# Performance work log

Hardware: AMD Instinct MI355X
Metric: run time of the kernel (lower is better)

Reference implementation:

```python
import jax, jax.numpy as jnp
import numpy as np

N = 50000      # nodes
E = 800000     # edges (avg degree 16)
IN, EMB, HID, OUT = 128, 256, 256, 128
KS = (25000, 12500)  # absolute top-k node counts per pooling level
NEG = -1e9


def setup_inputs() -> dict:
    key = jax.random.key(0)
    k = jax.random.split(key, 20)
    s = 0.05
    rn = lambda kk, shp: (jax.random.normal(kk, shp, jnp.float32) * s)
    return {
        "features": jax.random.normal(k[0], (N, IN), jnp.float32),
        "src": jax.random.randint(k[1], (E,), 0, N, dtype=jnp.int32),
        "dst": jax.random.randint(k[2], (E,), 0, N, dtype=jnp.int32),
        "W_embed": rn(k[3], (IN, EMB)), "b_embed": jnp.zeros((EMB,), jnp.float32),
        "W_enc0": rn(k[4], (EMB, HID)), "b_enc0": jnp.zeros((HID,), jnp.float32),
        "W_enc1": rn(k[5], (HID, HID)), "b_enc1": jnp.zeros((HID,), jnp.float32),
        "W_p0": rn(k[6], (HID, 1)), "b_p0": jnp.zeros((1,), jnp.float32),
        "W_p1": rn(k[7], (HID, 1)), "b_p1": jnp.zeros((1,), jnp.float32),
        "W_bot": rn(k[8], (HID, HID)), "b_bot": jnp.zeros((HID,), jnp.float32),
        "W_dec0": rn(k[9], (HID, HID)), "b_dec0": jnp.zeros((HID,), jnp.float32),
        "W_dec1": rn(k[10], (HID, OUT)), "b_dec1": jnp.zeros((OUT,), jnp.float32),
    }


def _gcn(h, src, dst, emask, W, b, act):
    """DGL GraphConv, norm='both': D_out^{-1/2} A D_in^{-1/2} h W + b, deg clamped >=1.
    emask: float [E] validity mask for edges of the current (sub)graph."""
    n = h.shape[0]
    deg_out = jnp.clip(jax.ops.segment_sum(emask, src, num_segments=n), 1.0)
    deg_in = jnp.clip(jax.ops.segment_sum(emask, dst, num_segments=n), 1.0)
    msg = (h * (deg_out ** -0.5)[:, None])[src] * emask[:, None]  # [E, F]
    agg = jax.ops.segment_sum(msg, dst, num_segments=n)
    out = (agg * (deg_in ** -0.5)[:, None]) @ W + b
    return jax.nn.relu(out) if act else out


def _forward(features, src, dst, W_embed, b_embed, W_enc0, b_enc0, W_enc1, b_enc1,
             W_p0, b_p0, W_p1, b_p1, W_bot, b_bot, W_dec0, b_dec0, W_dec1, b_dec1):
    n = features.shape[0]
    ones_e = jnp.ones((src.shape[0],), features.dtype)
    enc = [(W_enc0, b_enc0), (W_enc1, b_enc1)]
    pools = [(W_p0, b_p0), (W_p1, b_p1)]
    dec = [(W_dec0, b_dec0), (W_dec1, b_dec1)]
    L = len(KS)

    h = _gcn(features, src, dst, ones_e, W_embed, b_embed, True)
    masks = [jnp.ones((n,), features.dtype)]  # node mask per graph level
    hidden = []
    for i in range(L):  # encoder (dropout = eval-mode identity)
        m = masks[i]
        em = m[src] * m[dst]
        h = _gcn(h, src, dst, em, enc[i][0], enc[i][1], True) * m[:, None]
        hidden.append(h)
        # gPool: sigmoid projection score, top-k node selection, gate by score
        scores = jax.nn.sigmoid(h @ pools[i][0] + pools[i][1])[:, 0]
        _, idx = jax.lax.top_k(jnp.where(m > 0, scores, NEG), KS[i])
        nm = jnp.zeros((n,), features.dtype).at[idx].set(1.0)
        h = h * (scores * nm)[:, None]
        masks.append(nm)
    mL = masks[L]
    emL = mL[src] * mL[dst]
    h = _gcn(h, src, dst, emL, W_bot, b_bot, True) * mL[:, None]
    for i in range(L):  # decoder: gUnpool (identity under full-rep masking) + skip + GCN
        j = L - 1 - i
        h = h + hidden[j]
        m = masks[j]
        em = m[src] * m[dst]
        act = i < L - 1  # last decoder layer has no activation
        h = _gcn(h, src, dst, em, dec[i][0], dec[i][1], act) * m[:, None]
    return h


def reference(features, src, dst, W_embed, b_embed, W_enc0, b_enc0, W_enc1, b_enc1,
              W_p0, b_p0, W_p1, b_p1, W_bot, b_bot, W_dec0, b_dec0, W_dec1, b_dec1):
    return _forward(features, src, dst, W_embed, b_embed, W_enc0, b_enc0, W_enc1, b_enc1,
                    W_p0, b_p0, W_p1, b_p1, W_bot, b_bot, W_dec0, b_dec0, W_dec1, b_dec1)
```

## Files before the change

kernel.cpp:

```cpp
#include <hip/hip_runtime.h>
#include <hip/hip_bf16.h>
#include <type_traits>

__global__ void hist_kernel(const int* __restrict__ src, const int* __restrict__ dst,
                            int* __restrict__ deg_out, int* __restrict__ deg_in, int E) {
    int e = blockIdx.x * blockDim.x + threadIdx.x;
    if (e < E) {
        atomicAdd(&deg_out[src[e]], 1);
        atomicAdd(&deg_in[dst[e]], 1);
    }
}

__global__ void scan_kernel(const int* __restrict__ deg, int* __restrict__ row_ptr,
                            int* __restrict__ cursor, int n) {
    __shared__ int wsum[16];
    __shared__ int running;
    int tid = threadIdx.x, lane = tid & 63, wid = tid >> 6;
    if (tid == 0) running = 0;
    __syncthreads();
    for (int base = 0; base < n; base += 1024) {
        int i = base + tid;
        int v = (i < n) ? deg[i] : 0;
        int incl = v;
        #pragma unroll
        for (int off = 1; off < 64; off <<= 1) {
            int t = __shfl_up(incl, off);
            if (lane >= off) incl += t;
        }
        if (lane == 63) wsum[wid] = incl;
        __syncthreads();
        if (wid == 0 && lane < 16) {
            int s = wsum[lane], si = s;
            #pragma unroll
            for (int off = 1; off < 16; off <<= 1) {
                int t = __shfl_up(si, off);
                if (lane >= off) si += t;
            }
            wsum[lane] = si - s;
        }
        __syncthreads();
        int excl = running + wsum[wid] + (incl - v);
        if (i < n) { row_ptr[i] = excl; cursor[i] = excl; }
        __syncthreads();
        if (tid == 1023) running = excl + v;
        __syncthreads();
    }
    if (tid == 0) row_ptr[n] = running;
}

__global__ void fill_kernel(const int* __restrict__ src, const int* __restrict__ dst,
                            int* __restrict__ cursor, int* __restrict__ col, int E) {
    int e = blockIdx.x * blockDim.x + threadIdx.x;
    if (e < E) {
        int p = atomicAdd(&cursor[dst[e]], 1);
        col[p] = src[e];
    }
}

__global__ void sort_rows_kernel(const int* __restrict__ row_ptr, int* __restrict__ col, int n) {
    int v = blockIdx.x * blockDim.x + threadIdx.x;
    if (v >= n) return;
    int e0 = row_ptr[v], e1 = row_ptr[v + 1];
    for (int i = e0 + 1; i < e1; ++i) {
        int key = col[i];
        int j = i - 1;
        while (j >= e0 && col[j] > key) { col[j + 1] = col[j]; --j; }
        col[j + 1] = key;
    }
}

__global__ void out_deg_mask_kernel(const int* __restrict__ src, const int* __restrict__ dst,
                                    const float* __restrict__ m, float* __restrict__ so, int E) {
    int e = blockIdx.x * blockDim.x + threadIdx.x;
    if (e < E) {
        float md = m[dst[e]];
        if (md != 0.f) atomicAdd(&so[src[e]], md);
    }
}

__global__ void in_deg_mask_kernel(const int* __restrict__ row_ptr, const int* __restrict__ col,
                                   const float* __restrict__ m, float* __restrict__ si, int n) {
    int v = blockIdx.x * blockDim.x + threadIdx.x;
    if (v < n) {
        float s = 0.f;
        int e1 = row_ptr[v + 1];
        for (int e = row_ptr[v]; e < e1; ++e) s += m[col[e]];
        si[v] = s;
    }
}

__global__ void scale_full_kernel(const int* __restrict__ dout, const int* __restrict__ din,
                                  float* __restrict__ s, float* __restrict__ t, int n) {
    int v = blockIdx.x * blockDim.x + threadIdx.x;
    if (v < n) {
        s[v] = 1.f / sqrtf((float)max(dout[v], 1));
        t[v] = 1.f / sqrtf((float)max(din[v], 1));
    }
}

__global__ void scale_mask_kernel(const float* __restrict__ gate, const float* __restrict__ mask,
                                  const float* __restrict__ so, const float* __restrict__ si,
                                  float* __restrict__ s, float* __restrict__ t, int n) {
    int v = blockIdx.x * blockDim.x + threadIdx.x;
    if (v < n) {
        s[v] = gate[v] * (1.f / sqrtf(fmaxf(so[v], 1.f)));
        t[v] = mask[v] * (1.f / sqrtf(fmaxf(si[v], 1.f)));
    }
}

__global__ void agg_feat_128_kernel(const int* __restrict__ row_ptr, const int* __restrict__ col,
                                    const float* __restrict__ X, const float* __restrict__ s,
                                    const float* __restrict__ t, float* __restrict__ out, int n) {
    int tid = threadIdx.x;
    int node = blockIdx.x * 8 + (tid >> 5);
    int f4 = tid & 31;
    if (node >= n) return;
    int e0 = row_ptr[node], e1 = row_ptr[node + 1];
    const float4* X4 = (const float4*)X;
    float ax = 0.f, ay = 0.f, az = 0.f, aw = 0.f;
    int e = e0;
    for (; e + 3 < e1; e += 4) {
        int u0 = col[e], u1 = col[e + 1], u2 = col[e + 2], u3 = col[e + 3];
        float s0 = s[u0], s1 = s[u1], s2 = s[u2], s3 = s[u3];
        float4 x0 = X4[(size_t)u0 * 32 + f4];
        float4 x1 = X4[(size_t)u1 * 32 + f4];
        float4 x2 = X4[(size_t)u2 * 32 + f4];
        float4 x3 = X4[(size_t)u3 * 32 + f4];
        ax += s0 * x0.x; ay += s0 * x0.y; az += s0 * x0.z; aw += s0 * x0.w;
        ax += s1 * x1.x; ay += s1 * x1.y; az += s1 * x1.z; aw += s1 * x1.w;
        ax += s2 * x2.x; ay += s2 * x2.y; az += s2 * x2.z; aw += s2 * x2.w;
        ax += s3 * x3.x; ay += s3 * x3.y; az += s3 * x3.z; aw += s3 * x3.w;
    }
    for (; e < e1; ++e) {
        int u = col[e];
        float sc = s[u];
        float4 q = X4[(size_t)u * 32 + f4];
        ax += sc * q.x; ay += sc * q.y; az += sc * q.z; aw += sc * q.w;
    }
    float tv = t[node];
    float4 r; r.x = ax * tv; r.y = ay * tv; r.z = az * tv; r.w = aw * tv;
    ((float4*)out)[(size_t)node * 32 + f4] = r;
}

template <bool MASKED>
__global__ void agg_f32_256_kernel(const int* __restrict__ row_ptr, const int* __restrict__ col,
                                   const float* __restrict__ X, const float* __restrict__ s,
                                   const float* __restrict__ t, float* __restrict__ out, int n) {
    int tid = threadIdx.x;
    int node = blockIdx.x * 4 + (tid >> 6);
    int f4 = tid & 63;
    if (node >= n) return;
    float tv = t[node];
    if (MASKED && tv == 0.f) return;
    int e0 = row_ptr[node], e1 = row_ptr[node + 1];
    const float4* X4 = (const float4*)X;
    float ax = 0.f, ay = 0.f, az = 0.f, aw = 0.f;
    int e = e0;
    for (; e + 3 < e1; e += 4) {
        int u0 = col[e], u1 = col[e + 1], u2 = col[e + 2], u3 = col[e + 3];
        float s0 = s[u0], s1 = s[u1], s2 = s[u2], s3 = s[u3];
        if (!MASKED) {
            float4 x0 = X4[(size_t)u0 * 64 + f4];
            float4 x1 = X4[(size_t)u1 * 64 + f4];
            float4 x2 = X4[(size_t)u2 * 64 + f4];
            float4 x3 = X4[(size_t)u3 * 64 + f4];
            ax += s0 * x0.x; ay += s0 * x0.y; az += s0 * x0.z; aw += s0 * x0.w;
            ax += s1 * x1.x; ay += s1 * x1.y; az += s1 * x1.z; aw += s1 * x1.w;
            ax += s2 * x2.x; ay += s2 * x2.y; az += s2 * x2.z; aw += s2 * x2.w;
            ax += s3 * x3.x; ay += s3 * x3.y; az += s3 * x3.z; aw += s3 * x3.w;
        } else {
            if (s0 != 0.f) { float4 x = X4[(size_t)u0 * 64 + f4];
                ax += s0 * x.x; ay += s0 * x.y; az += s0 * x.z; aw += s0 * x.w; }
            if (s1 != 0.f) { float4 x = X4[(size_t)u1 * 64 + f4];
                ax += s1 * x.x; ay += s1 * x.y; az += s1 * x.z; aw += s1 * x.w; }
            if (s2 != 0.f) { float4 x = X4[(size_t)u2 * 64 + f4];
                ax += s2 * x.x; ay += s2 * x.y; az += s2 * x.z; aw += s2 * x.w; }
            if (s3 != 0.f) { float4 x = X4[(size_t)u3 * 64 + f4];
                ax += s3 * x.x; ay += s3 * x.y; az += s3 * x.z; aw += s3 * x.w; }
        }
    }
    for (; e < e1; ++e) {
        int u = col[e];
        float sc = s[u];
        if (!MASKED || sc != 0.f) {
            float4 xv = X4[(size_t)u * 64 + f4];
            ax += sc * xv.x; ay += sc * xv.y; az += sc * xv.z; aw += sc * xv.w;
        }
    }
    float4 r; r.x = ax * tv; r.y = ay * tv; r.z = az * tv; r.w = aw * tv;
    ((float4*)out)[(size_t)node * 64 + f4] = r;
}

__global__ void agg_bias_128_kernel(const int* __restrict__ row_ptr, const int* __restrict__ col,
                                    const float* __restrict__ P, const float* __restrict__ t,
                                    const float* __restrict__ bias, float* __restrict__ out, int n) {
    int tid = threadIdx.x;
    int node = blockIdx.x * 8 + (tid >> 5);
    int f4 = tid & 31;
    if (node >= n) return;
    int e0 = row_ptr[node], e1 = row_ptr[node + 1];
    const float4* P4 = (const float4*)P;
    float ax = 0.f, ay = 0.f, az = 0.f, aw = 0.f;
    int e = e0;
    for (; e + 3 < e1; e += 4) {
        int u0 = col[e], u1 = col[e + 1], u2 = col[e + 2], u3 = col[e + 3];
        float4 x0 = P4[(size_t)u0 * 32 + f4];
        float4 x1 = P4[(size_t)u1 * 32 + f4];
        float4 x2 = P4[(size_t)u2 * 32 + f4];
        float4 x3 = P4[(size_t)u3 * 32 + f4];
        ax += x0.x; ay += x0.y; az += x0.z; aw += x0.w;
        ax += x1.x; ay += x1.y; az += x1.z; aw += x1.w;
        ax += x2.x; ay += x2.y; az += x2.z; aw += x2.w;
        ax += x3.x; ay += x3.y; az += x3.z; aw += x3.w;
    }
    for (; e < e1; ++e) {
        int u = col[e];
        float4 q = P4[(size_t)u * 32 + f4];
        ax += q.x; ay += q.y; az += q.z; aw += q.w;
    }
    float tv = t[node];
    float4 bv = ((const float4*)bias)[f4];
    float4 r;
    r.x = ax * tv + bv.x; r.y = ay * tv + bv.y;
    r.z = az * tv + bv.z; r.w = aw * tv + bv.w;
    ((float4*)out)[(size_t)node * 32 + f4] = r;
}

template <bool RELU>
__global__ __launch_bounds__(256) void gemm_kernel(const float* __restrict__ A,
                                                   const float* __restrict__ W,
                                                   const float* __restrict__ bias,
                                                   const float* __restrict__ mask,
                                                   const float* __restrict__ rowscale,
                                                   float* __restrict__ C, int M, int K, int Nn) {
    __shared__ float As[16][68];
    __shared__ float Bs[16][68];
    int tid = threadIdx.x;
    int bm = blockIdx.x * 64, bn = blockIdx.y * 64;
    int mA = tid >> 2, kqA = (tid & 3) * 4;
    int kB = tid >> 4, nqB = (tid & 15) * 4;
    int tn = (tid & 15) * 4, tm = (tid >> 4) * 4;
    float acc[4][4] = {};
    float rs = rowscale ? rowscale[bm + mA] : 1.f;
    for (int k0 = 0; k0 < K; k0 += 16) {
        float4 av = *(const float4*)(A + (size_t)(bm + mA) * K + k0 + kqA);
        As[kqA + 0][mA] = av.x * rs; As[kqA + 1][mA] = av.y * rs;
        As[kqA + 2][mA] = av.z * rs; As[kqA + 3][mA] = av.w * rs;
        float4 bv = *(const float4*)(W + (size_t)(k0 + kB) * Nn + bn + nqB);
        *(float4*)&Bs[kB][nqB] = bv;
        __syncthreads();
        #pragma unroll
        for (int kk = 0; kk < 16; ++kk) {
            float4 a = *(const float4*)&As[kk][tm];
            float4 b = *(const float4*)&Bs[kk][tn];
            float ar[4] = {a.x, a.y, a.z, a.w};
            float br[4] = {b.x, b.y, b.z, b.w};
            #pragma unroll
            for (int i2 = 0; i2 < 4; i2++)
                #pragma unroll
                for (int j = 0; j < 4; j++) acc[i2][j] += ar[i2] * br[j];
        }
        __syncthreads();
    }
    #pragma unroll
    for (int i2 = 0; i2 < 4; i2++) {
        int row = bm + tm + i2;
        if (row < M) {
            float mv = mask ? mask[row] : 1.f;
            #pragma unroll
            for (int j = 0; j < 4; j++) {
                float x = acc[i2][j] + (bias ? bias[bn + tn + j] : 0.f);
                if (RELU) x = fmaxf(x, 0.f);
                x *= mv;
                C[(size_t)row * Nn + bn + tn + j] = x;
            }
        }
    }
}

template <bool RELU>
__global__ __launch_bounds__(256) void gemm_rows_kernel(const float* __restrict__ A,
                                                        const float* __restrict__ W,
                                                        const float* __restrict__ bias,
                                                        const int* __restrict__ idx, int Mc,
                                                        float* __restrict__ C, int K, int Nn) {
    __shared__ float As[16][68];
    __shared__ float Bs[16][68];
    __shared__ int ridx[64];
    int tid = threadIdx.x;
    int bm = blockIdx.x * 64, bn = blockIdx.y * 64;
    if (tid < 64) {
        int r = bm + tid;
        ridx[tid] = (r < Mc) ? idx[r] : idx[0];
    }
    __syncthreads();
    int mA = tid >> 2, kqA = (tid & 3) * 4;
    int kB = tid >> 4, nqB = (tid & 15) * 4;
    int tn = (tid & 15) * 4, tm = (tid >> 4) * 4;
    int rA = ridx[mA];
    float acc[4][4] = {};
    for (int k0 = 0; k0 < K; k0 += 16) {
        float4 av = *(const float4*)(A + (size_t)rA * K + k0 + kqA);
        As[kqA + 0][mA] = av.x; As[kqA + 1][mA] = av.y;
        As[kqA + 2][mA] = av.z; As[kqA + 3][mA] = av.w;
        float4 bv = *(const float4*)(W + (size_t)(k0 + kB) * Nn + bn + nqB);
        *(float4*)&Bs[kB][nqB] = bv;
        __syncthreads();
        #pragma unroll
        for (int kk = 0; kk < 16; ++kk) {
            float4 a = *(const float4*)&As[kk][tm];
            float4 b = *(const float4*)&Bs[kk][tn];
            float ar[4] = {a.x, a.y, a.z, a.w};
            float br[4] = {b.x, b.y, b.z, b.w};
            #pragma unroll
            for (int i2 = 0; i2 < 4; i2++)
                #pragma unroll
                for (int j = 0; j < 4; j++) acc[i2][j] += ar[i2] * br[j];
        }
        __syncthreads();
    }
    #pragma unroll
    for (int i2 = 0; i2 < 4; i2++) {
        int r = bm + tm + i2;
        if (r < Mc) {
            int row = ridx[tm + i2];
            #pragma unroll
            for (int j = 0; j < 4; j++) {
                float x = acc[i2][j] + bias[bn + tn + j];
                if (RELU) x = fmaxf(x, 0.f);
                C[(size_t)row * Nn + bn + tn + j] = x;
            }
        }
    }
}

__global__ void score_kernel(const float* __restrict__ H, const float* __restrict__ Wp,
                             const float* __restrict__ bp, const float* __restrict__ mask,
                             float* __restrict__ scores, float* __restrict__ keys, int n) {
    int lane = threadIdx.x & 63;
    int node = blockIdx.x * 4 + (threadIdx.x >> 6);
    if (node >= n) return;
    float4 hv = ((const float4*)(H + (size_t)node * 256))[lane];
    float4 wq = ((const float4*)Wp)[lane];
    float d = hv.x * wq.x + hv.y * wq.y + hv.z * wq.z + hv.w * wq.w;
    #pragma unroll
    for (int off = 32; off > 0; off >>= 1) d += __shfl_down(d, off);
    if (lane == 0) {
        float sc = 1.f / (1.f + expf(-(d + bp[0])));
        scores[node] = sc;
        keys[node] = (mask && mask[node] == 0.f) ? -1e9f : sc;
    }
}

__device__ __forceinline__ unsigned key_u(float f) {
    unsigned u = __float_as_uint(f);
    return (u & 0x80000000u) ? ~u : (u | 0x80000000u);
}

__device__ __forceinline__ void wave_hist_add(int* __restrict__ hist, unsigned bin, bool valid) {
    int lane = threadIdx.x & 63;
    while (true) {
        unsigned long long vmask = __ballot(valid);
        if (vmask == 0ull) break;
        int leader = __ffsll((long long)vmask) - 1;
        unsigned lbin = (unsigned)__shfl((int)bin, leader);
        bool match = valid && (bin == lbin);
        unsigned long long mmask = __ballot(match);
        if (lane == leader) atomicAdd(&hist[lbin], __popcll(mmask));
        if (match) valid = false;
    }
}

__global__ void topk_kernel(const float* __restrict__ keys, const float* __restrict__ scores,
                            float* __restrict__ nm, float* __restrict__ gate, int n, int K) {
    __shared__ int hist[256];
    __shared__ unsigned sh_prefix;
    __shared__ int sh_krem;
    __shared__ int sh_running;
    __shared__ int wsum[16];
    int tid = threadIdx.x, lane = tid & 63, wid = tid >> 6;
    if (tid == 0) { sh_prefix = 0u; sh_krem = K; sh_running = 0; }
    __syncthreads();
    for (int pass = 0; pass < 4; ++pass) {
        int shift = 24 - pass * 8;
        if (tid < 256) hist[tid] = 0;
        __syncthreads();
        unsigned pmask = (pass == 0) ? 0u : (0xFFFFFFFFu << (shift + 8));
        unsigned prefix = sh_prefix;
        for (int i = tid; i < n; i += 1024) {
            unsigned u = key_u(keys[i]);
            if ((u & pmask) == prefix) atomicAdd(&hist[(u >> shift) & 0xFF], 1);
        }
        __syncthreads();
        if (tid == 0) {
            int krem = sh_krem;
            int b;
            for (b = 255; b > 0; --b) {
                int c = hist[b];
                if (c >= krem) break;
                krem -= c;
            }
            sh_prefix = prefix | ((unsigned)b << shift);
            sh_krem = krem;
        }
        __syncthreads();
    }
    unsigned Tkey = sh_prefix;
    int need_eq = sh_krem;
    for (int base = 0; base < n; base += 1024) {
        int i = base + tid;
        unsigned u = 0; int flagv = 0;
        if (i < n) { u = key_u(keys[i]); flagv = (u == Tkey) ? 1 : 0; }
        unsigned long long bal = __ballot(flagv);
        int rank_w = __popcll(bal & ((1ull << lane) - 1ull));
        if (lane == 63) wsum[wid] = __popcll(bal);
        __syncthreads();
        int woff = 0;
        for (int w = 0; w < wid; ++w) woff += wsum[w];
        int grank = sh_running + woff + rank_w;
        if (i < n) {
            float v = (u > Tkey) ? 1.f : ((flagv && grank < need_eq) ? 1.f : 0.f);
            nm[i] = v;
            gate[i] = v * scores[i];
        }
        __syncthreads();
        if (tid == 0) {
            int tot = 0;
            for (int w = 0; w < 16; ++w) tot += wsum[w];
            sh_running += tot;
        }
        __syncthreads();
    }
}

__global__ void topk_hist1(const float* __restrict__ keys, int n, int* __restrict__ hist) {
    int i = blockIdx.x * blockDim.x + threadIdx.x;
    unsigned bin = 0; bool valid = (i < n);
    if (valid) bin = key_u(keys[i]) >> 16;
    wave_hist_add(hist, bin, valid);
}

__global__ void topk_scan1(const int* __restrict__ hist, int K, int* __restrict__ sel) {
    __shared__ int arr[1024];
    int tid = threadIdx.x;
    int base = tid * 64;
    int local = 0;
    #pragma unroll 8
    for (int b = 0; b < 64; ++b) local += hist[base + b];
    arr[tid] = local;
    __syncthreads();
    for (int off = 1; off < 1024; off <<= 1) {
        int v = (tid + off < 1024) ? arr[tid + off] : 0;
        __syncthreads();
        arr[tid] += v;
        __syncthreads();
    }
    int above = arr[tid] - local;
    if (above < K && arr[tid] >= K) {
        int run = above;
        for (int b = base + 63; b >= base; --b) {
            int c = hist[b];
            if (run + c >= K) { sel[0] = b; sel[1] = K - run; break; }
            run += c;
        }
    }
}

__global__ void topk_hist2(const float* __restrict__ keys, int n, const int* __restrict__ sel,
                           int* __restrict__ hist) {
    int i = blockIdx.x * blockDim.x + threadIdx.x;
    unsigned bin = 0; bool valid = false;
    if (i < n) {
        unsigned u = key_u(keys[i]);
        if ((int)(u >> 16) == sel[0]) { bin = u & 0xFFFF; valid = true; }
    }
    wave_hist_add(hist, bin, valid);
}

__global__ void topk_scan2(const int* __restrict__ hist, int* __restrict__ sel,
                           int* __restrict__ tie_cnt) {
    __shared__ int arr[1024];
    int tid = threadIdx.x;
    if (tid == 0) *tie_cnt = 0;
    int K = sel[1];
    int base = tid * 64;
    int local = 0;
    #pragma unroll 8
    for (int b = 0; b < 64; ++b) local += hist[base + b];
    arr[tid] = local;
    __syncthreads();
    for (int off = 1; off < 1024; off <<= 1) {
        int v = (tid + off < 1024) ? arr[tid + off] : 0;
        __syncthreads();
        arr[tid] += v;
        __syncthreads();
    }
    int above = arr[tid] - local;
    if (above < K && arr[tid] >= K) {
        int run = above;
        for (int b = base + 63; b >= base; --b) {
            int c = hist[b];
            if (run + c >= K) {
                sel[2] = (int)((((unsigned)sel[0]) << 16) | (unsigned)b);
                sel[3] = K - run;
                break;
            }
            run += c;
        }
    }
}

__global__ void topk_mark(const float* __restrict__ keys, const float* __restrict__ scores,
                          const int* __restrict__ sel, float* __restrict__ nm,
                          float* __restrict__ gate, int* __restrict__ tie_list,
                          int* __restrict__ tie_cnt, int n) {
    int i = blockIdx.x * blockDim.x + threadIdx.x;
    if (i >= n) return;
    unsigned Tkey = (unsigned)sel[2];
    unsigned u = key_u(keys[i]);
    float v = 0.f;
    if (u > Tkey) v = 1.f;
    else if (u == Tkey) { int p = atomicAdd(tie_cnt, 1); tie_list[p] = i; }
    nm[i] = v;
    gate[i] = v * scores[i];
}

__global__ void topk_ties(const float* __restrict__ scores, const int* __restrict__ sel,
                          const int* __restrict__ tie_list, const int* __restrict__ tie_cnt,
                          float* __restrict__ nm, float* __restrict__ gate) {
    int cnt = *tie_cnt;
    int need = sel[3];
    for (int j = threadIdx.x; j < cnt; j += blockDim.x) {
        int idx = tie_list[j];
        int rank = 0;
        for (int k2 = 0; k2 < cnt; ++k2) rank += (tie_list[k2] < idx) ? 1 : 0;
        if (rank < need) { nm[idx] = 1.f; gate[idx] = scores[idx]; }
    }
}

__global__ void compact_kernel(const float* __restrict__ nm, int* __restrict__ idx,
                               int* __restrict__ cnt, int n) {
    int i = blockIdx.x * blockDim.x + threadIdx.x;
    if (i < n && nm[i] != 0.f) {
        int p = atomicAdd(cnt, 1);
        idx[p] = i;
    }
}

__global__ void add_mask_kernel(float* __restrict__ A, const float* __restrict__ B,
                                const float* __restrict__ mask, int n4) {
    int i = blockIdx.x * blockDim.x + threadIdx.x;
    if (i < n4) {
        float4 a = ((float4*)A)[i];
        float4 b = ((const float4*)B)[i];
        if (mask && mask[i >> 6] == 0.f) { a.x = 0.f; a.y = 0.f; a.z = 0.f; a.w = 0.f; }
        a.x += b.x; a.y += b.y; a.z += b.z; a.w += b.w;
        ((float4*)A)[i] = a;
    }
}

extern "C" void kernel_launch(void* const* d_in, const int* in_sizes, int n_in,
                              void* d_out, int out_size, void* d_ws, size_t ws_size,
                              hipStream_t stream) {
    const int n = in_sizes[0] / 128;
    const int E = in_sizes[1];
    const int NPAD = ((n + 63) / 64) * 64;
    const int K1 = 25000, K2 = 12500;

    const float* features = (const float*)d_in[0];
    const int* src = (const int*)d_in[1];
    const int* dst = (const int*)d_in[2];
    const float* W_embed = (const float*)d_in[3];
    const float* b_embed = (const float*)d_in[4];
    const float* W_enc0  = (const float*)d_in[5];
    const float* b_enc0  = (const float*)d_in[6];
    const float* W_enc1  = (const float*)d_in[7];
    const float* b_enc1  = (const float*)d_in[8];
    const float* W_p0    = (const float*)d_in[9];
    const float* b_p0    = (const float*)d_in[10];
    const float* W_p1    = (const float*)d_in[11];
    const float* b_p1    = (const float*)d_in[12];
    const float* W_bot   = (const float*)d_in[13];
    const float* b_bot   = (const float*)d_in[14];
    const float* W_dec0  = (const float*)d_in[15];
    const float* b_dec0  = (const float*)d_in[16];
    const float* W_dec1  = (const float*)d_in[17];
    const float* b_dec1  = (const float*)d_in[18];
    float* out_f = (float*)d_out;

    char* ws = (char*)d_ws;
    size_t off = 0;
    auto alloc = [&](size_t bytes) -> void* {
        void* p = ws + off;
        off += (bytes + 255) & ~(size_t)255;
        return p;
    };
    (void)alloc(256);
    int* row_ptr  = (int*)alloc((size_t)(n + 1) * 4);
    int* cursor   = (int*)alloc((size_t)n * 4);
    int* col      = (int*)alloc((size_t)E * 4);
    int* deg_out_i= (int*)alloc((size_t)n * 4);
    int* deg_in_i = (int*)alloc((size_t)n * 4);
    float* so_m1  = (float*)alloc((size_t)n * 4);
    float* si_m1  = (float*)alloc((size_t)n * 4);
    float* so_m2  = (float*)alloc((size_t)n * 4);
    float* si_m2  = (float*)alloc((size_t)n * 4);
    float* sarr   = (float*)alloc((size_t)n * 4);
    float* tarr   = (float*)alloc((size_t)n * 4);
    float* scores1= (float*)alloc((size_t)n * 4);
    float* keys1  = (float*)alloc((size_t)n * 4);
    float* scores2= (float*)alloc((size_t)n * 4);
    float* keys2  = (float*)alloc((size_t)n * 4);
    float* nm1    = (float*)alloc((size_t)n * 4);
    float* gate1  = (float*)alloc((size_t)n * 4);
    float* nm2    = (float*)alloc((size_t)n * 4);
    float* gate2  = (float*)alloc((size_t)n * 4);
    size_t big = (size_t)NPAD * 256 * 4;
    float* A = (float*)alloc(big);
    float* B = (float*)alloc(big);
    float* C = (float*)alloc(big);
    float* D = (float*)alloc(big);
    int* rhist    = (int*)alloc(65536 * 4);
    int* sel      = (int*)alloc(256);
    int* tie_cnt  = (int*)alloc(256);
    int* tie_list = (int*)alloc((size_t)n * 4);
    float* s0     = (float*)alloc((size_t)n * 4);
    float* t0     = (float*)alloc((size_t)n * 4);
    int* idx1     = (int*)alloc((size_t)n * 4);
    int* idx2     = (int*)alloc((size_t)n * 4);
    int* ccnt     = (int*)alloc(256);
    bool fast = (off <= ws_size);

    dim3 blk(256);
    int gE = (E + 255) / 256;
    int gN = (n + 255) / 256;
    int gAgg256 = (n + 3) / 4;
    int gAgg128 = (n + 7) / 8;
    int gScore = (n + 3) / 4;
    dim3 gemm_g(NPAD / 64, 4);
    dim3 gemm_g128(NPAD / 64, 2);
    dim3 gemm_gK1((K1 + 63) / 64, 4);
    dim3 gemm_gK2((K2 + 63) / 64, 4);
    int gAdd = (n * 64 + 255) / 256;

    auto run_topk = [&](const float* keys, const float* scores, float* nm, float* gate, int K) {
        if (fast) {
            hipMemsetAsync(rhist, 0, 65536 * 4, stream);
            topk_hist1<<<gN, blk, 0, stream>>>(keys, n, rhist);
            topk_scan1<<<1, 1024, 0, stream>>>(rhist, K, sel);
            hipMemsetAsync(rhist, 0, 65536 * 4, stream);
            topk_hist2<<<gN, blk, 0, stream>>>(keys, n, sel, rhist);
            topk_scan2<<<1, 1024, 0, stream>>>(rhist, sel, tie_cnt);
            topk_mark<<<gN, blk, 0, stream>>>(keys, scores, sel, nm, gate, tie_list, tie_cnt, n);
            topk_ties<<<1, 256, 0, stream>>>(scores, sel, tie_list, tie_cnt, nm, gate);
        } else {
            topk_kernel<<<1, 1024, 0, stream>>>(keys, scores, nm, gate, n, K);
        }
    };
    float* sF = fast ? s0 : sarr;
    float* tF = fast ? t0 : tarr;

    hipMemsetAsync(deg_out_i, 0, (size_t)n * 4, stream);
    hipMemsetAsync(deg_in_i, 0, (size_t)n * 4, stream);
    hist_kernel<<<gE, blk, 0, stream>>>(src, dst, deg_out_i, deg_in_i, E);
    scan_kernel<<<1, 1024, 0, stream>>>(deg_in_i, row_ptr, cursor, n);
    fill_kernel<<<gE, blk, 0, stream>>>(src, dst, cursor, col, E);
    sort_rows_kernel<<<gN, blk, 0, stream>>>(row_ptr, col, n);

    scale_full_kernel<<<gN, blk, 0, stream>>>(deg_out_i, deg_in_i, sF, tF, n);

    agg_feat_128_kernel<<<gAgg128, blk, 0, stream>>>(row_ptr, col, features, sF, tF, D, n);
    gemm_kernel<true><<<gemm_g, blk, 0, stream>>>(D, W_embed, b_embed, nullptr, nullptr, A, n, 128, 256);

    agg_f32_256_kernel<false><<<gAgg256, blk, 0, stream>>>(row_ptr, col, A, sF, tF, D, n);
    gemm_kernel<true><<<gemm_g, blk, 0, stream>>>(D, W_enc0, b_enc0, nullptr, nullptr, B, n, 256, 256);

    score_kernel<<<gScore, blk, 0, stream>>>(B, W_p0, b_p0, nullptr, scores1, keys1, n);
    run_topk(keys1, scores1, nm1, gate1, K1);
    if (fast) {
        hipMemsetAsync(ccnt, 0, 4, stream);
        compact_kernel<<<gN, blk, 0, stream>>>(nm1, idx1, ccnt, n);
    }

    hipMemsetAsync(so_m1, 0, (size_t)n * 4, stream);
    out_deg_mask_kernel<<<gE, blk, 0, stream>>>(src, dst, nm1, so_m1, E);
    in_deg_mask_kernel<<<gN, blk, 0, stream>>>(row_ptr, col, nm1, si_m1, n);
    scale_mask_kernel<<<gN, blk, 0, stream>>>(gate1, nm1, so_m1, si_m1, sarr, tarr, n);
    agg_f32_256_kernel<true><<<gAgg256, blk, 0, stream>>>(row_ptr, col, B, sarr, tarr, D, n);
    if (fast)
        gemm_rows_kernel<true><<<gemm_gK1, blk, 0, stream>>>(D, W_enc1, b_enc1, idx1, K1, C, 256, 256);
    else
        gemm_kernel<true><<<gemm_g, blk, 0, stream>>>(D, W_enc1, b_enc1, nm1, nullptr, C, n, 256, 256);

    score_kernel<<<gScore, blk, 0, stream>>>(C, W_p1, b_p1, nm1, scores2, keys2, n);
    run_topk(keys2, scores2, nm2, gate2, K2);
    if (fast) {
        hipMemsetAsync(ccnt + 1, 0, 4, stream);
        compact_kernel<<<gN, blk, 0, stream>>>(nm2, idx2, ccnt + 1, n);
    }

    hipMemsetAsync(so_m2, 0, (size_t)n * 4, stream);
    out_deg_mask_kernel<<<gE, blk, 0, stream>>>(src, dst, nm2, so_m2, E);
    in_deg_mask_kernel<<<gN, blk, 0, stream>>>(row_ptr, col, nm2, si_m2, n);
    scale_mask_kernel<<<gN, blk, 0, stream>>>(gate2, nm2, so_m2, si_m2, sarr, tarr, n);
    agg_f32_256_kernel<true><<<gAgg256, blk, 0, stream>>>(row_ptr, col, C, sarr, tarr, D, n);
    if (fast)
        gemm_rows_kernel<true><<<gemm_gK2, blk, 0, stream>>>(D, W_bot, b_bot, idx2, K2, A, 256, 256);
    else
        gemm_kernel<true><<<gemm_g, blk, 0, stream>>>(D, W_bot, b_bot, nm2, nullptr, A, n, 256, 256);

    add_mask_kernel<<<gAdd, blk, 0, stream>>>(A, C, fast ? nm2 : nullptr, n * 64);
    scale_mask_kernel<<<gN, blk, 0, stream>>>(nm1, nm1, so_m1, si_m1, sarr, tarr, n);
    agg_f32_256_kernel<true><<<gAgg256, blk, 0, stream>>>(row_ptr, col, A, sarr, tarr, D, n);
    if (fast)
        gemm_rows_kernel<true><<<gemm_gK1, blk, 0, stream>>>(D, W_dec0, b_dec0, idx1, K1, A, 256, 256);
    else
        gemm_kernel<true><<<gemm_g, blk, 0, stream>>>(D, W_dec0, b_dec0, nm1, nullptr, A, n, 256, 256);

    add_mask_kernel<<<gAdd, blk, 0, stream>>>(A, B, fast ? nm1 : nullptr, n * 64);
    if (!fast)
        scale_full_kernel<<<gN, blk, 0, stream>>>(deg_out_i, deg_in_i, sarr, tarr, n);
    gemm_kernel<false><<<gemm_g128, blk, 0, stream>>>(A, W_dec1, nullptr, nullptr, sF, C, n, 256, 128);
    agg_bias_128_kernel<<<gAgg128, blk, 0, stream>>>(row_ptr, col, C, tF, b_dec1, out_f, n);

    (void)n_in; (void)out_size;
}
```

Baseline: 1.313 ms.

## Widen GEMM tiles to 64x128 with 4x8 register micro-tiles per thread

```diff
diff --git a/kernel.cpp b/kernel.cpp
--- a/kernel.cpp
+++ b/kernel.cpp
@@ -234,31 +234,33 @@
                                                    const float* __restrict__ rowscale,
                                                    float* __restrict__ C, int M, int K, int Nn) {
     __shared__ float As[16][68];
-    __shared__ float Bs[16][68];
+    __shared__ float Bs[16][132];
     int tid = threadIdx.x;
-    int bm = blockIdx.x * 64, bn = blockIdx.y * 64;
+    int bm = blockIdx.x * 64, bn = blockIdx.y * 128;
     int mA = tid >> 2, kqA = (tid & 3) * 4;
-    int kB = tid >> 4, nqB = (tid & 15) * 4;
-    int tn = (tid & 15) * 4, tm = (tid >> 4) * 4;
-    float acc[4][4] = {};
+    int kB = tid >> 4, nqB = (tid & 15) * 8;
+    int tm = (tid >> 4) * 4, tn = (tid & 15) * 4;
+    float acc[4][8] = {};
     float rs = rowscale ? rowscale[bm + mA] : 1.f;
     for (int k0 = 0; k0 < K; k0 += 16) {
         float4 av = *(const float4*)(A + (size_t)(bm + mA) * K + k0 + kqA);
         As[kqA + 0][mA] = av.x * rs; As[kqA + 1][mA] = av.y * rs;
         As[kqA + 2][mA] = av.z * rs; As[kqA + 3][mA] = av.w * rs;
-        float4 bv = *(const float4*)(W + (size_t)(k0 + kB) * Nn + bn + nqB);
-        *(float4*)&Bs[kB][nqB] = bv;
+        const float* wp = W + (size_t)(k0 + kB) * Nn + bn + nqB;
+        *(float4*)&Bs[kB][nqB]     = *(const float4*)wp;
+        *(float4*)&Bs[kB][nqB + 4] = *(const float4*)(wp + 4);
         __syncthreads();
         #pragma unroll
         for (int kk = 0; kk < 16; ++kk) {
-            float4 a = *(const float4*)&As[kk][tm];
-            float4 b = *(const float4*)&Bs[kk][tn];
+            float4 a  = *(const float4*)&As[kk][tm];
+            float4 b0 = *(const float4*)&Bs[kk][tn];
+            float4 b1 = *(const float4*)&Bs[kk][tn + 64];
             float ar[4] = {a.x, a.y, a.z, a.w};
-            float br[4] = {b.x, b.y, b.z, b.w};
+            float br[8] = {b0.x, b0.y, b0.z, b0.w, b1.x, b1.y, b1.z, b1.w};
             #pragma unroll
             for (int i2 = 0; i2 < 4; i2++)
                 #pragma unroll
-                for (int j = 0; j < 4; j++) acc[i2][j] += ar[i2] * br[j];
+                for (int j = 0; j < 8; j++) acc[i2][j] += ar[i2] * br[j];
         }
         __syncthreads();
     }
@@ -267,13 +269,17 @@
         int row = bm + tm + i2;
         if (row < M) {
             float mv = mask ? mask[row] : 1.f;
+            float o[8];
             #pragma unroll
-            for (int j = 0; j < 4; j++) {
-                float x = acc[i2][j] + (bias ? bias[bn + tn + j] : 0.f);
+            for (int j = 0; j < 8; j++) {
+                int cj = (j < 4) ? (tn + j) : (64 + tn + j - 4);
+                float x = acc[i2][j] + (bias ? bias[bn + cj] : 0.f);
                 if (RELU) x = fmaxf(x, 0.f);
-                x *= mv;
-                C[(size_t)row * Nn + bn + tn + j] = x;
+                o[j] = x * mv;
             }
+            float* cp = C + (size_t)row * Nn + bn;
+            *(float4*)(cp + tn)      = make_float4(o[0], o[1], o[2], o[3]);
+            *(float4*)(cp + 64 + tn) = make_float4(o[4], o[5], o[6], o[7]);
         }
     }
 }
@@ -285,37 +291,39 @@
                                                         const int* __restrict__ idx, int Mc,
                                                         float* __restrict__ C, int K, int Nn) {
     __shared__ float As[16][68];
-    __shared__ float Bs[16][68];
+    __shared__ float Bs[16][132];
     __shared__ int ridx[64];
     int tid = threadIdx.x;
-    int bm = blockIdx.x * 64, bn = blockIdx.y * 64;
+    int bm = blockIdx.x * 64, bn = blockIdx.y * 128;
     if (tid < 64) {
         int r = bm + tid;
         ridx[tid] = (r < Mc) ? idx[r] : idx[0];
     }
     __syncthreads();
     int mA = tid >> 2, kqA = (tid & 3) * 4;
-    int kB = tid >> 4, nqB = (tid & 15) * 4;
-    int tn = (tid & 15) * 4, tm = (tid >> 4) * 4;
+    int kB = tid >> 4, nqB = (tid & 15) * 8;
+    int tm = (tid >> 4) * 4, tn = (tid & 15) * 4;
     int rA = ridx[mA];
-    float acc[4][4] = {};
+    float acc[4][8] = {};
     for (int k0 = 0; k0 < K; k0 += 16) {
         float4 av = *(const float4*)(A + (size_t)rA * K + k0 + kqA);
         As[kqA + 0][mA] = av.x; As[kqA + 1][mA] = av.y;
         As[kqA + 2][mA] = av.z; As[kqA + 3][mA] = av.w;
-        float4 bv = *(const float4*)(W + (size_t)(k0 + kB) * Nn + bn + nqB);
-        *(float4*)&Bs[kB][nqB] = bv;
+        const float* wp = W + (size_t)(k0 + kB) * Nn + bn + nqB;
+        *(float4*)&Bs[kB][nqB]     = *(const float4*)wp;
+        *(float4*)&Bs[kB][nqB + 4] = *(const float4*)(wp + 4);
         __syncthreads();
         #pragma unroll
         for (int kk = 0; kk < 16; ++kk) {
-            float4 a = *(const float4*)&As[kk][tm];
-            float4 b = *(const float4*)&Bs[kk][tn];
+            float4 a  = *(const float4*)&As[kk][tm];
+            float4 b0 = *(const float4*)&Bs[kk][tn];
+            float4 b1 = *(const float4*)&Bs[kk][tn + 64];
             float ar[4] = {a.x, a.y, a.z, a.w};
-            float br[4] = {b.x, b.y, b.z, b.w};
+            float br[8] = {b0.x, b0.y, b0.z, b0.w, b1.x, b1.y, b1.z, b1.w};
             #pragma unroll
             for (int i2 = 0; i2 < 4; i2++)
                 #pragma unroll
-                for (int j = 0; j < 4; j++) acc[i2][j] += ar[i2] * br[j];
+                for (int j = 0; j < 8; j++) acc[i2][j] += ar[i2] * br[j];
         }
         __syncthreads();
     }
@@ -324,12 +332,17 @@
         int r = bm + tm + i2;
         if (r < Mc) {
             int row = ridx[tm + i2];
+            float o[8];
             #pragma unroll
-            for (int j = 0; j < 4; j++) {
-                float x = acc[i2][j] + bias[bn + tn + j];
+            for (int j = 0; j < 8; j++) {
+                int cj = (j < 4) ? (tn + j) : (64 + tn + j - 4);
+                float x = acc[i2][j] + bias[bn + cj];
                 if (RELU) x = fmaxf(x, 0.f);
-                C[(size_t)row * Nn + bn + tn + j] = x;
+                o[j] = x;
             }
+            float* cp = C + (size_t)row * Nn + bn;
+            *(float4*)(cp + tn)      = make_float4(o[0], o[1], o[2], o[3]);
+            *(float4*)(cp + 64 + tn) = make_float4(o[4], o[5], o[6], o[7]);
         }
     }
 }
@@ -637,10 +650,10 @@
     int gAgg256 = (n + 3) / 4;
     int gAgg128 = (n + 7) / 8;
     int gScore = (n + 3) / 4;
-    dim3 gemm_g(NPAD / 64, 4);
-    dim3 gemm_g128(NPAD / 64, 2);
-    dim3 gemm_gK1((K1 + 63) / 64, 4);
-    dim3 gemm_gK2((K2 + 63) / 64, 4);
+    dim3 gemm_g(NPAD / 64, 2);
+    dim3 gemm_g128(NPAD / 64, 1);
+    dim3 gemm_gK1((K1 + 63) / 64, 2);
+    dim3 gemm_gK2((K2 + 63) / 64, 2);
     int gAdd = (n * 64 + 255) / 256;
 
     auto run_topk = [&](const float* keys, const float* scores, float* nm, float* gate, int K) {
```

Measured after the change: 1.312 ms. Within noise of the previous version (-0.1%).
